# Kernel optimization log

Measured on AMD Instinct MI355X. Metric: run time of the kernel, lower is better.

Reference implementation:

```python
import jax, jax.numpy as jnp
import numpy as np

EYE_PENALTY = 1.0e6


def setup_inputs() -> dict:
    key = jax.random.key(0)
    k1, k2 = jax.random.split(key)
    B, NIN, NK, DK = 512, 1024, 128, 5
    x = jax.random.normal(k1, (B, NIN), dtype=jnp.float32)
    theta = jax.random.normal(k2, (NIN, NK, DK), dtype=jnp.float32) * 0.05
    log_weight_scale = jnp.zeros((NK, DK), dtype=jnp.float32)
    bias = jnp.full((NK,), -1.0, dtype=jnp.float32)
    return {"x": x, "theta": theta, "log_weight_scale": log_weight_scale, "bias": bias}


def reference(x, theta, log_weight_scale, bias):
    # kernel = theta * exp(log_weight_scale) / ||theta||_2 (norm over input dim)
    l2 = jnp.sqrt(jnp.sum(theta * theta, axis=0))            # [K, D]
    kernel = theta * (jnp.exp(log_weight_scale) / l2)[None]   # [NIN, K, D]
    actv = jnp.einsum('bi,ikd->bkd', x, kernel)               # [B, K, D]
    B = x.shape[0]
    # all-pairs L1 distance per kernel: [B, K, B]
    diff = actv[:, :, :, None] - jnp.transpose(actv, (1, 2, 0))[None]  # [B,K,D,B]
    abs_dif = jnp.sum(jnp.abs(diff), axis=2)                  # [B, K, B]
    abs_dif = abs_dif + EYE_PENALTY * jnp.eye(B, dtype=x.dtype)[:, None, :]
    f = jnp.sum(jnp.exp(-abs_dif), axis=2) + bias[None, :]    # [B, K]
    return jnp.concatenate([x, f], axis=1)                    # [B, NIN + K]
```

## Files before the change

### kernel.cpp

```cpp
#include <hip/hip_runtime.h>
#include <hip/hip_fp16.h>
#include <math.h>

constexpr int B    = 512;
constexpr int NIN  = 1024;
constexpr int NK   = 128;
constexpr int DK   = 5;
constexpr int NF   = NK * DK;
constexpr int NOUT = NIN + NK;
constexpr int SPLITK = 8;
constexpr int LDA = 136;
#define LOG2E 1.44269504088896f

typedef _Float16 f16x2 __attribute__((ext_vector_type(2)));
typedef _Float16 f16x4 __attribute__((ext_vector_type(4)));
typedef _Float16 f16x8 __attribute__((ext_vector_type(8)));
typedef float    f32x4 __attribute__((ext_vector_type(4)));

union H2 { __half2 h; f16x2 v; unsigned u; };

__global__ __launch_bounds__(256) void gemm_kernel(
        const float* __restrict__ x,
        const float* __restrict__ theta,
        float* __restrict__ actvP,
        float* __restrict__ ps) {
    __shared__ _Float16 Ath[64 * LDA];
    __shared__ _Float16 Bxh[64 * LDA];
    __shared__ float    red2[16][64];

    const int t    = threadIdx.x;
    const int tile = blockIdx.x >> 3;
    const int z    = blockIdx.x & 7;
    const int n0   = (tile >> 3) * 64;
    const int b0   = (tile & 7) * 64;
    const bool do_ps = (tile & 7) == 0;
    const int kw   = z * 128;

    const int kq  = t >> 4;
    const int tn4 = (t & 15) * 4;
    float4 tv[8];
    #pragma unroll
    for (int i = 0; i < 8; ++i)
        tv[i] = *(const float4*)&theta[(kw + kq * 8 + i) * NF + n0 + tn4];

    const int br = t >> 2;
    const int ki = t & 3;
    float4 xv[8];
    #pragma unroll
    for (int i = 0; i < 8; ++i)
        xv[i] = *(const float4*)&x[(b0 + br) * NIN + kw + (ki + i * 4) * 4];

    if (do_ps) {
        float sq0 = 0.f, sq1 = 0.f, sq2 = 0.f, sq3 = 0.f;
        #pragma unroll
        for (int i = 0; i < 8; ++i) {
            sq0 += tv[i].x * tv[i].x;  sq1 += tv[i].y * tv[i].y;
            sq2 += tv[i].z * tv[i].z;  sq3 += tv[i].w * tv[i].w;
        }
        red2[kq][tn4 + 0] = sq0;  red2[kq][tn4 + 1] = sq1;
        red2[kq][tn4 + 2] = sq2;  red2[kq][tn4 + 3] = sq3;
    }

    {
        f16x8 h;
        #pragma unroll
        for (int i = 0; i < 8; ++i) h[i] = (_Float16)tv[i].x;
        *(f16x8*)&Ath[(tn4 + 0) * LDA + kq * 8] = h;
        #pragma unroll
        for (int i = 0; i < 8; ++i) h[i] = (_Float16)tv[i].y;
        *(f16x8*)&Ath[(tn4 + 1) * LDA + kq * 8] = h;
        #pragma unroll
        for (int i = 0; i < 8; ++i) h[i] = (_Float16)tv[i].z;
        *(f16x8*)&Ath[(tn4 + 2) * LDA + kq * 8] = h;
        #pragma unroll
        for (int i = 0; i < 8; ++i) h[i] = (_Float16)tv[i].w;
        *(f16x8*)&Ath[(tn4 + 3) * LDA + kq * 8] = h;
    }
    #pragma unroll
    for (int i = 0; i < 8; ++i) {
        f16x4 h;
        h[0] = (_Float16)xv[i].x;  h[1] = (_Float16)xv[i].y;
        h[2] = (_Float16)xv[i].z;  h[3] = (_Float16)xv[i].w;
        *(f16x4*)&Bxh[br * LDA + (ki + i * 4) * 4] = h;
    }
    __syncthreads();

    const int w   = t >> 6;
    const int l   = t & 63;
    const int r16 = l & 15;
    const int kg  = l >> 4;

    f32x4 acc0 = {0.f,0.f,0.f,0.f}, acc1 = {0.f,0.f,0.f,0.f};
    f32x4 acc2 = {0.f,0.f,0.f,0.f}, acc3 = {0.f,0.f,0.f,0.f};
    #pragma unroll
    for (int ks = 0; ks < 4; ++ks) {
        const f16x8 av  = *(const f16x8*)&Ath[(w*16 + r16)*LDA + ks*32 + kg*8];
        const f16x8 bv0 = *(const f16x8*)&Bxh[( 0 + r16)*LDA + ks*32 + kg*8];
        const f16x8 bv1 = *(const f16x8*)&Bxh[(16 + r16)*LDA + ks*32 + kg*8];
        const f16x8 bv2 = *(const f16x8*)&Bxh[(32 + r16)*LDA + ks*32 + kg*8];
        const f16x8 bv3 = *(const f16x8*)&Bxh[(48 + r16)*LDA + ks*32 + kg*8];
        acc0 = __builtin_amdgcn_mfma_f32_16x16x32_f16(av, bv0, acc0, 0, 0, 0);
        acc1 = __builtin_amdgcn_mfma_f32_16x16x32_f16(av, bv1, acc1, 0, 0, 0);
        acc2 = __builtin_amdgcn_mfma_f32_16x16x32_f16(av, bv2, acc2, 0, 0, 0);
        acc3 = __builtin_amdgcn_mfma_f32_16x16x32_f16(av, bv3, acc3, 0, 0, 0);
    }

    {
        float* dst = actvP + (size_t)z * NF * B
                   + (size_t)(n0 + w*16 + kg*4) * B + b0 + r16;
        #pragma unroll
        for (int j = 0; j < 4; ++j) {
            dst[j*B +  0] = acc0[j];
            dst[j*B + 16] = acc1[j];
            dst[j*B + 32] = acc2[j];
            dst[j*B + 48] = acc3[j];
        }
    }
    if (do_ps) {
        __syncthreads();
        if (t < 64) {
            float tot = 0.f;
            #pragma unroll
            for (int rr = 0; rr < 16; ++rr) tot += red2[rr][t];
            ps[z * NF + n0 + t] = tot;
        }
    }
}

__global__ __launch_bounds__(256) void rs_kernel(
        const float* __restrict__ actvP,
        const float* __restrict__ ps,
        const float* __restrict__ lws,
        __half* __restrict__ actv16) {
    const int t   = threadIdx.x;
    const int row = blockIdx.x * 2 + (t >> 7);
    const int c4  = (t & 127) * 4;

    float nrm = 0.f;
    #pragma unroll
    for (int zz = 0; zz < SPLITK; ++zz) nrm += ps[zz * NF + row];
    const float s = __expf(lws[row]) * rsqrtf(nrm) * LOG2E;

    const float* p = actvP + (size_t)row * B + c4;
    float4 vs = *(const float4*)(p);
    #pragma unroll
    for (int zz = 1; zz < SPLITK; ++zz) {
        const float4 v = *(const float4*)(p + (size_t)zz * NF * B);
        vs.x += v.x; vs.y += v.y; vs.z += v.z; vs.w += v.w;
    }
    f16x4 h;
    h[0] = (_Float16)(vs.x * s);
    h[1] = (_Float16)(vs.y * s);
    h[2] = (_Float16)(vs.z * s);
    h[3] = (_Float16)(vs.w * s);
    *(f16x4*)&actv16[(size_t)row * B + c4] = h;
}

__global__ __launch_bounds__(256) void pairwise_kernel(
        const __half* __restrict__ actv16,
        const float* __restrict__ bias,
        const float* __restrict__ x,
        float* __restrict__ out) {
    __shared__ __half a16s[DK * B];
    __shared__ float  red[8 * 64];

    const int k = blockIdx.x;
    const int e = blockIdx.y;
    const int t = threadIdx.x;

    if (e < 4) {
        const int row = k * 4 + e;
        ((float4*)out)[row * (NOUT/4) + t] = ((const float4*)x)[row * (NIN/4) + t];
    }

    {
        const uint4* src = (const uint4*)(actv16 + (size_t)k * DK * B);
        ((uint4*)a16s)[t] = src[t];
        if (t < 64) ((uint4*)a16s)[256 + t] = src[256 + t];
    }
    __syncthreads();

    const int g  = t >> 5;
    const int r  = t & 31;
    const int ba = e * 64 + r;
    const int bb = ba + 32;

    __half2 A2[DK], B2[DK];
    #pragma unroll
    for (int d = 0; d < DK; ++d) {
        A2[d] = __half2half2(a16s[d * B + ba]);
        B2[d] = __half2half2(a16s[d * B + bb]);
    }
    const H2 ones = {__half2half2(__float2half(1.0f))};

    float accA = 0.f, accB = 0.f;
    const int bp0 = g * 64;

    union W8 { f16x8 v; __half2 h[4]; };
    #pragma unroll 2
    for (int m = 0; m < 8; ++m) {
        const int bp = bp0 + m * 8;
        W8 w0, w1, w2, w3, w4;
        w0.v = *(const f16x8*)&a16s[0*B + bp];
        w1.v = *(const f16x8*)&a16s[1*B + bp];
        w2.v = *(const f16x8*)&a16s[2*B + bp];
        w3.v = *(const f16x8*)&a16s[3*B + bp];
        w4.v = *(const f16x8*)&a16s[4*B + bp];
        #pragma unroll
        for (int c = 0; c < 4; ++c) {
            __half2 dA = __habs2(__hsub2(A2[0], w0.h[c]));
            dA = __hadd2(dA, __habs2(__hsub2(A2[1], w1.h[c])));
            dA = __hadd2(dA, __habs2(__hsub2(A2[2], w2.h[c])));
            dA = __hadd2(dA, __habs2(__hsub2(A2[3], w3.h[c])));
            dA = __hadd2(dA, __habs2(__hsub2(A2[4], w4.h[c])));
            H2 eA; eA.h = h2exp2(__hneg2(dA));
            __half2 dB = __habs2(__hsub2(B2[0], w0.h[c]));
            dB = __hadd2(dB, __habs2(__hsub2(B2[1], w1.h[c])));
            dB = __hadd2(dB, __habs2(__hsub2(B2[2], w2.h[c])));
            dB = __hadd2(dB, __habs2(__hsub2(B2[3], w3.h[c])));
            dB = __hadd2(dB, __habs2(__hsub2(B2[4], w4.h[c])));
            H2 eB; eB.h = h2exp2(__hneg2(dB));
#if __has_builtin(__builtin_amdgcn_fdot2)
            accA = __builtin_amdgcn_fdot2(eA.v, ones.v, accA, false);
            accB = __builtin_amdgcn_fdot2(eB.v, ones.v, accB, false);
#else
            accA += __low2float(eA.h) + __high2float(eA.h);
            accB += __low2float(eB.h) + __high2float(eB.h);
#endif
        }
    }
    red[g * 64 + r]      = accA;
    red[g * 64 + 32 + r] = accB;
    __syncthreads();
    if (t < 64) {
        float f = -1.0f + bias[k];
        #pragma unroll
        for (int gg = 0; gg < 8; ++gg) f += red[gg * 64 + t];
        out[(e * 64 + t) * NOUT + NIN + k] = f;
    }
}

extern "C" void kernel_launch(void* const* d_in, const int* in_sizes, int n_in,
                              void* d_out, int out_size, void* d_ws, size_t ws_size,
                              hipStream_t stream) {
    const float* x     = (const float*)d_in[0];
    const float* theta = (const float*)d_in[1];
    const float* lws   = (const float*)d_in[2];
    const float* bias  = (const float*)d_in[3];
    float* out = (float*)d_out;

    char* wsb = (char*)d_ws;
    float*  ps     = (float*)wsb;
    float*  actvP  = (float*)(wsb + (64 << 10));
    __half* actv16 = (__half*)(wsb + (64 << 10)
                               + (size_t)SPLITK * sizeof(float) * NF * B);

    gemm_kernel<<<dim3(640), 256, 0, stream>>>(x, theta, actvP, ps);
    rs_kernel<<<dim3(320), 256, 0, stream>>>(actvP, ps, lws, actv16);
    pairwise_kernel<<<dim3(NK, 8), 256, 0, stream>>>(actv16, bias, x, out);
}
```

Measured before the change: 28.44 us.

## Fuse split-K reduction and scaling into pairwise kernel, store partials as fp16

```diff
diff --git a/kernel.cpp b/kernel.cpp
--- a/kernel.cpp
+++ b/kernel.cpp
@@ -22,7 +22,7 @@
 __global__ __launch_bounds__(256) void gemm_kernel(
         const float* __restrict__ x,
         const float* __restrict__ theta,
-        float* __restrict__ actvP,
+        __half* __restrict__ actvP16,
         float* __restrict__ ps) {
     __shared__ _Float16 Ath[64 * LDA];
     __shared__ _Float16 Bxh[64 * LDA];
@@ -106,14 +106,14 @@
     }
 
     {
-        float* dst = actvP + (size_t)z * NF * B
-                   + (size_t)(n0 + w*16 + kg*4) * B + b0 + r16;
+        __half* dst = actvP16 + (size_t)z * NF * B
+                    + (size_t)(n0 + w*16 + kg*4) * B + b0 + r16;
         #pragma unroll
         for (int j = 0; j < 4; ++j) {
-            dst[j*B +  0] = acc0[j];
-            dst[j*B + 16] = acc1[j];
-            dst[j*B + 32] = acc2[j];
-            dst[j*B + 48] = acc3[j];
+            dst[j*B +  0] = __float2half(acc0[j]);
+            dst[j*B + 16] = __float2half(acc1[j]);
+            dst[j*B + 32] = __float2half(acc2[j]);
+            dst[j*B + 48] = __float2half(acc3[j]);
         }
     }
     if (do_ps) {
@@ -127,42 +127,17 @@
     }
 }
 
-__global__ __launch_bounds__(256) void rs_kernel(
-        const float* __restrict__ actvP,
+__global__ __launch_bounds__(256) void pairwise_kernel(
+        const __half* __restrict__ actvP16,
         const float* __restrict__ ps,
         const float* __restrict__ lws,
-        __half* __restrict__ actv16) {
-    const int t   = threadIdx.x;
-    const int row = blockIdx.x * 2 + (t >> 7);
-    const int c4  = (t & 127) * 4;
-
-    float nrm = 0.f;
-    #pragma unroll
-    for (int zz = 0; zz < SPLITK; ++zz) nrm += ps[zz * NF + row];
-    const float s = __expf(lws[row]) * rsqrtf(nrm) * LOG2E;
-
-    const float* p = actvP + (size_t)row * B + c4;
-    float4 vs = *(const float4*)(p);
-    #pragma unroll
-    for (int zz = 1; zz < SPLITK; ++zz) {
-        const float4 v = *(const float4*)(p + (size_t)zz * NF * B);
-        vs.x += v.x; vs.y += v.y; vs.z += v.z; vs.w += v.w;
-    }
-    f16x4 h;
-    h[0] = (_Float16)(vs.x * s);
-    h[1] = (_Float16)(vs.y * s);
-    h[2] = (_Float16)(vs.z * s);
-    h[3] = (_Float16)(vs.w * s);
-    *(f16x4*)&actv16[(size_t)row * B + c4] = h;
-}
-
-__global__ __launch_bounds__(256) void pairwise_kernel(
-        const __half* __restrict__ actv16,
         const float* __restrict__ bias,
         const float* __restrict__ x,
         float* __restrict__ out) {
     __shared__ __half a16s[DK * B];
     __shared__ float  red[8 * 64];
+    __shared__ float  s_sh[DK];
+    __shared__ float  red_ps[DK * SPLITK];
 
     const int k = blockIdx.x;
     const int e = blockIdx.y;
@@ -173,10 +148,49 @@
         ((float4*)out)[row * (NOUT/4) + t] = ((const float4*)x)[row * (NIN/4) + t];
     }
 
-    {
-        const uint4* src = (const uint4*)(actv16 + (size_t)k * DK * B);
-        ((uint4*)a16s)[t] = src[t];
-        if (t < 64) ((uint4*)a16s)[256 + t] = src[256 + t];
+    if (t < DK * SPLITK)
+        red_ps[t] = ps[(t / DK) * NF + k * DK + (t % DK)];
+
+    const size_t slab = (size_t)k * DK * B;
+    float acc0f[8], acc1f[8];
+    {
+        #pragma unroll
+        for (int i = 0; i < 8; ++i) { acc0f[i] = 0.f; acc1f[i] = 0.f; }
+        #pragma unroll
+        for (int z = 0; z < SPLITK; ++z) {
+            const f16x8 v = *(const f16x8*)(actvP16 + (size_t)z * NF * B + slab + t * 8);
+            #pragma unroll
+            for (int i = 0; i < 8; ++i) acc0f[i] += (float)v[i];
+        }
+        if (t < 64) {
+            #pragma unroll
+            for (int z = 0; z < SPLITK; ++z) {
+                const f16x8 v = *(const f16x8*)(actvP16 + (size_t)z * NF * B + slab + 2048 + t * 8);
+                #pragma unroll
+                for (int i = 0; i < 8; ++i) acc1f[i] += (float)v[i];
+            }
+        }
+    }
+    __syncthreads();
+    if (t < DK) {
+        float sum = 0.f;
+        #pragma unroll
+        for (int c = 0; c < SPLITK; ++c) sum += red_ps[c * DK + t];
+        s_sh[t] = __expf(lws[k * DK + t]) * rsqrtf(sum) * LOG2E;
+    }
+    __syncthreads();
+    {
+        const float s0 = s_sh[t >> 6];
+        f16x8 h;
+        #pragma unroll
+        for (int i = 0; i < 8; ++i) h[i] = (_Float16)(acc0f[i] * s0);
+        *(f16x8*)&a16s[t * 8] = h;
+        if (t < 64) {
+            const float s1 = s_sh[4];
+            #pragma unroll
+            for (int i = 0; i < 8; ++i) h[i] = (_Float16)(acc1f[i] * s1);
+            *(f16x8*)&a16s[2048 + t * 8] = h;
+        }
     }
     __syncthreads();
 
@@ -250,12 +264,9 @@
     float* out = (float*)d_out;
 
     char* wsb = (char*)d_ws;
-    float*  ps     = (float*)wsb;
-    float*  actvP  = (float*)(wsb + (64 << 10));
-    __half* actv16 = (__half*)(wsb + (64 << 10)
-                               + (size_t)SPLITK * sizeof(float) * NF * B);
-
-    gemm_kernel<<<dim3(640), 256, 0, stream>>>(x, theta, actvP, ps);
-    rs_kernel<<<dim3(320), 256, 0, stream>>>(actvP, ps, lws, actv16);
-    pairwise_kernel<<<dim3(NK, 8), 256, 0, stream>>>(actv16, bias, x, out);
+    float*  ps       = (float*)wsb;
+    __half* actvP16  = (__half*)(wsb + (64 << 10));
+
+    gemm_kernel<<<dim3(640), 256, 0, stream>>>(x, theta, actvP16, ps);
+    pairwise_kernel<<<dim3(NK, 8), 256, 0, stream>>>(actvP16, ps, lws, bias, x, out);
 }
```

New measurement: 24.82 us. -12.7%, faster.
